# Optimization experiments

Measured on AMD Instinct MI355X. Metric: run time of the kernel, lower is better.

Reference implementation:

```python
import jax, jax.numpy as jnp
import numpy as np

K = 3
STRIDE = 1
PAD = 1
DIL = 1


def setup_inputs() -> dict:
    key = jax.random.key(0)
    k1, k2, k3, k4 = jax.random.split(key, 4)
    B, C, H, W = 8, 64, 96, 96
    O = 64
    x = jax.random.normal(k1, (B, C, H, W), jnp.float32)
    # offset-predicting conv is conventionally near-zero init -> small offsets
    w_off = jax.random.normal(k2, (2 * K * K, C, K, K), jnp.float32) * 0.01
    b_off = jax.random.normal(k3, (2 * K * K,), jnp.float32) * 0.01
    w_dcn = jax.random.normal(k4, (O, C, K, K), jnp.float32) * (1.0 / np.sqrt(C * K * K))
    return {"x": x, "w_off": w_off, "b_off": b_off, "w_dcn": w_dcn}


def _deform_conv(x, offset, w_dcn):
    B, C, H, W = x.shape
    O = w_dcn.shape[0]
    Ho, Wo = offset.shape[2], offset.shape[3]
    K2 = K * K
    # torchvision layout: offset[:, 2*k] = dy, offset[:, 2*k+1] = dx, k = ky*K + kx
    off = offset.reshape(B, K2, 2, Ho, Wo)
    kk = jnp.arange(K2)
    ky = (kk // K).astype(jnp.float32)
    kx = (kk % K).astype(jnp.float32)
    base_h = (jnp.arange(Ho) * STRIDE - PAD).astype(jnp.float32)
    base_w = (jnp.arange(Wo) * STRIDE - PAD).astype(jnp.float32)
    # sampling positions, shape [B, K2, Ho, Wo]
    py = off[:, :, 0] + base_h[None, None, :, None] + (ky * DIL)[None, :, None, None]
    px = off[:, :, 1] + base_w[None, None, None, :] + (kx * DIL)[None, :, None, None]

    y0 = jnp.floor(py)
    x0 = jnp.floor(px)
    wy = py - y0
    wx = px - x0
    y0i = y0.astype(jnp.int32)
    x0i = x0.astype(jnp.int32)
    y1i = y0i + 1
    x1i = x0i + 1

    x_flat = x.reshape(B, C, H * W)
    N = K2 * Ho * Wo

    def gather(yi, xi):
        valid = (yi >= 0) & (yi < H) & (xi >= 0) & (xi < W)
        lin = jnp.clip(yi, 0, H - 1) * W + jnp.clip(xi, 0, W - 1)  # [B,K2,Ho,Wo]
        idx = jnp.broadcast_to(lin.reshape(B, 1, N), (B, C, N))
        v = jnp.take_along_axis(x_flat, idx, axis=2).reshape(B, C, K2, Ho, Wo)
        return v * valid[:, None].astype(x.dtype)

    w00 = ((1 - wy) * (1 - wx))[:, None]
    w01 = ((1 - wy) * wx)[:, None]
    w10 = (wy * (1 - wx))[:, None]
    w11 = (wy * wx)[:, None]
    sampled = (gather(y0i, x0i) * w00 + gather(y0i, x1i) * w01
               + gather(y1i, x0i) * w10 + gather(y1i, x1i) * w11)  # [B,C,K2,Ho,Wo]

    # deformable conv = contraction over (c_in, kernel pos); bias=False
    return jnp.einsum('bckhw,ock->bohw', sampled, w_dcn.reshape(O, C, K2))


def reference(x, w_off, b_off, w_dcn):
    offset = jax.lax.conv_general_dilated(
        x, w_off, window_strides=(STRIDE, STRIDE), padding=[(PAD, PAD), (PAD, PAD)],
        rhs_dilation=(DIL, DIL), dimension_numbers=('NCHW', 'OIHW', 'NCHW'))
    offset = offset + b_off[None, :, None, None]
    return _deform_conv(x, offset, w_dcn)
```

## Files before the change

### kernel.cpp

```cpp
#include <hip/hip_runtime.h>

#define BB 8
#define CC 64
#define HH 96
#define WW 96
#define OO 64
#define KK 3
#define K2 9
#define HW (HH*WW)
#define NOFF 18
#define NPIX (BB*HW)
#define MT 64
#define NTILE (HW/MT)
#define NXCD 8
#define WR 6
#define WC 36
#define NWIN (WR*WC)
#define OSTR 21

typedef _Float16 f16;
typedef __attribute__((ext_vector_type(2))) _Float16 f16x2;
typedef __attribute__((ext_vector_type(4))) _Float16 f16x4;
typedef __attribute__((ext_vector_type(4))) float f32x4;
typedef __attribute__((ext_vector_type(2))) unsigned int uint2v;
typedef __attribute__((ext_vector_type(4))) unsigned int uint4v;

#define MFMA16(a,b,c) __builtin_amdgcn_mfma_f32_16x16x16f16(a,b,c,0,0,0)

__device__ __forceinline__ f16x2 bch(unsigned u) { return __builtin_bit_cast(f16x2, u); }
__device__ __forceinline__ unsigned bcu(f16x2 h) { return __builtin_bit_cast(unsigned, h); }
__device__ __forceinline__ f16x4 fq(unsigned a, unsigned b) {
  uint2v u = {a, b};
  return __builtin_bit_cast(f16x4, u);
}
__device__ __forceinline__ f16x4 fq2(uint2v u) { return __builtin_bit_cast(f16x4, u); }
__device__ __forceinline__ int xcd_remap(int bid, int per) {
  return (bid & 7) * per + (bid >> 3);
}

__global__ __launch_bounds__(256) void transpose_kernel(
    const float* __restrict__ x, unsigned short* __restrict__ xt) {
  int t = threadIdx.x;
  int px = xcd_remap(blockIdx.x, NPIX / 64 / NXCD) * 64 + (t & 63);
  int cg = t >> 6;
  int b = px / HW, hw = px % HW;
  const float* xp = x + (size_t)b * CC * HW + (size_t)(cg * 16) * HW + hw;
  f16 r[16];
  #pragma unroll
  for (int i = 0; i < 16; ++i) r[i] = (f16)xp[i * HW];
  uint4v v0, v1;
  #pragma unroll
  for (int q = 0; q < 4; ++q) {
    f16x2 a = {r[q*2], r[q*2+1]};       v0[q] = bcu(a);
    f16x2 bq = {r[8+q*2], r[8+q*2+1]};  v1[q] = bcu(bq);
  }
  uint4v* dst = (uint4v*)(xt + (size_t)px * CC + cg * 16);
  dst[0] = v0; dst[1] = v1;
}

__global__ void prep_kernel(const float* __restrict__ w_dcn,
                            const float* __restrict__ w_off,
                            unsigned short* __restrict__ wtx,
                            unsigned short* __restrict__ wofx) {
  int idx = blockIdx.x * 256 + threadIdx.x;
  if (idx < 36864) {
    int e = idx & 15;
    int l = (idx >> 4) & 63;
    int nb = (idx >> 10) & 3;
    int k = idx >> 12;
    int c = 16 * (l >> 4) + e;
    int o = nb * 16 + (l & 15);
    f16 h = (f16)w_dcn[(o * CC + c) * K2 + k];
    wtx[idx] = __builtin_bit_cast(unsigned short, h);
  } else {
    int i2 = idx - 36864;
    int e = i2 & 3;
    int l = (i2 >> 2) & 63;
    int q = (i2 >> 8) & 3;
    int n = (i2 >> 10) & 1;
    int kt = i2 >> 11;
    int c = q * 16 + 4 * (l >> 4) + e;
    int j = n * 16 + (l & 15);
    f16 h = (f16)((j < NOFF) ? w_off[(j * CC + c) * K2 + kt] : 0.f);
    wofx[i2] = __builtin_bit_cast(unsigned short, h);
  }
}

#define XWIN_OFF 0
#define OFFS_OFF 27648
#define ACCX_OFF 0
#define SMEM_SZ  33024

__global__ __launch_bounds__(512, 4) void fused_kernel(
    const unsigned short* __restrict__ xt,
    const unsigned short* __restrict__ wofx,
    const float* __restrict__ b_off,
    const unsigned short* __restrict__ wtx,
    float* __restrict__ out) {
  __shared__ __align__(16) char smem[SMEM_SZ];
  char* xwin = smem + XWIN_OFF;
  float* offs = (float*)(smem + OFFS_OFF);
  float* accx = (float*)(smem + ACCX_OFF);

  int t = threadIdx.x;
  int blk = xcd_remap(blockIdx.x, NPIX / MT / NXCD);
  int b = blk / NTILE;
  int ti = blk % NTILE;
  int tr = ti / 3, tc = ti % 3;
  int h0 = tr * 2, w0 = tc * 32;
  int hw0 = h0 * WW + w0;

  const char* xb = (const char*)(xt + (size_t)b * HW * CC);

  #pragma unroll
  for (int r = 0; r < 4; ++r) {
    int d = r * 512 + t;
    if (d < NWIN * 8) {
      int row = d >> 3, sg = d & 7;
      int wr_ = row / WC, wc_ = row - wr_ * WC;
      int gy = h0 - 2 + wr_;
      int gx = w0 - 2 + wc_;
      uint4v v = (uint4v){0u, 0u, 0u, 0u};
      if (((unsigned)gy < HH) && ((unsigned)gx < WW))
        v = *(const uint4v*)(xb + (size_t)((gy * WW + gx) << 7) + (sg << 4));
      *(uint4v*)&xwin[row * 128 + ((sg ^ (row & 7)) << 4)] = v;
    }
  }
  __syncthreads();

  int wv = t >> 6;
  int l  = t & 63;
  int lr = l & 15, lh = l >> 4;

  {
    int m = wv & 3, n = wv >> 2;
    int p = m * 16 + lr;
    int prow = ((p >> 5) + 1) * WC + (p & 31) + 1;
    f32x4 accO = (f32x4){0.f, 0.f, 0.f, 0.f};
    #pragma unroll
    for (int kt = 0; kt < K2; ++kt) {
      int wrow = prow + (kt / 3) * WC + (kt % 3);
      int rs = wrow & 7;
      const char* bp = (const char*)wofx + (((size_t)(kt * 2 + n) * 4) * 64 + l) * 8;
      #pragma unroll
      for (int q = 0; q < 4; ++q) {
        uint2v a2 = *(const uint2v*)&xwin[wrow * 128
                      + ((((q << 1) + (lh >> 1)) ^ rs) << 4) + ((lh & 1) << 3)];
        uint2v b2 = *(const uint2v*)(bp + (size_t)q * (64 * 8));
        accO = MFMA16(fq2(a2), fq2(b2), accO);
      }
    }
    int j = n * 16 + lr;
    if (j < NOFF) {
      float bj = b_off[j];
      #pragma unroll
      for (int r = 0; r < 4; ++r) {
        int px = m * 16 + lh * 4 + r;
        offs[px * OSTR + j] = accO[r] + bj;
      }
    }
  }
  __syncthreads();

  int grp = wv >> 2;
  int base = grp * 5;
  int cnt  = 5 - grp;
  int Ra = (wv & 3) * 16 + lr;
  int hpix = h0 + (Ra >> 5), wpix = w0 + (Ra & 31);
  int cB = lh * 32;

  unsigned po01[5], po23[5], pw01[5], pw23[5];
  unsigned emask = 0;
  #pragma unroll
  for (int i = 0; i < 5; ++i) {
    po01[i] = 0; po23[i] = 0; pw01[i] = 0; pw23[i] = 0;
    if (i < cnt) {
      int kt = base + i;
      int ky = kt / 3, kx = kt % 3;
      float py = offs[Ra * OSTR + 2 * kt]     + (float)(hpix - 1 + ky);
      float px = offs[Ra * OSTR + 2 * kt + 1] + (float)(wpix - 1 + kx);
      float y0f = floorf(py), x0f = floorf(px);
      float wy = py - y0f, wx = px - x0f;
      int y0 = (int)y0f, x0 = (int)x0f;
      int y1 = y0 + 1, x1 = x0 + 1;
      bool vy0 = (unsigned)y0 < HH, vy1 = (unsigned)y1 < HH;
      bool vx0 = (unsigned)x0 < WW, vx1 = (unsigned)x1 < WW;
      int cy0 = min(max(y0, 0), HH - 1), cy1 = min(max(y1, 0), HH - 1);
      int cx0 = min(max(x0, 0), WW - 1), cx1 = min(max(x1, 0), WW - 1);
      float g00 = (1.f - wy) * (1.f - wx) * ((vy0 && vx0) ? 1.f : 0.f);
      float g01 = (1.f - wy) * wx         * ((vy0 && vx1) ? 1.f : 0.f);
      float g10 = wy * (1.f - wx)         * ((vy1 && vx0) ? 1.f : 0.f);
      float g11 = wy * wx                 * ((vy1 && vx1) ? 1.f : 0.f);
      int ry0 = cy0 - (h0 - 2), ry1 = cy1 - (h0 - 2);
      int rx0 = cx0 - (w0 - 2), rx1 = cx1 - (w0 - 2);
      bool inw = ((unsigned)ry0 < WR) && ((unsigned)ry1 < WR) &&
                 ((unsigned)rx0 < WC) && ((unsigned)rx1 < WC);
      if (inw) {
        po01[i] = (unsigned)((ry0 * WC + rx0) << 7)
                | ((unsigned)((ry0 * WC + rx1) << 7) << 16);
        po23[i] = (unsigned)((ry1 * WC + rx0) << 7)
                | ((unsigned)((ry1 * WC + rx1) << 7) << 16);
      } else {
        po01[i] = (unsigned)(cy0 * WW + cx0)
                | ((unsigned)(cy0 * WW + cx1) << 16) | 0x80000000u;
        po23[i] = (unsigned)(cy1 * WW + cx0)
                | ((unsigned)(cy1 * WW + cx1) << 16);
        emask |= 1u << i;
      }
      f16x2 wa = {(f16)g00, (f16)g01};
      f16x2 wb = {(f16)g10, (f16)g11};
      pw01[i] = bcu(wa);
      pw23[i] = bcu(wb);
    }
  }

  f32x4 acc[4];
  #pragma unroll
  for (int nb = 0; nb < 4; ++nb) acc[nb] = (f32x4){0.f, 0.f, 0.f, 0.f};

  #define WREAD(bo, pos) (*(const uint4v*)&xwin[(bo) + ((pos) << 4)])
  if (__ballot(emask != 0) == 0ull) {
    #pragma unroll
    for (int i = 0; i < 5; ++i) {
      if (i < cnt) {
        unsigned e0 = po01[i], e1 = po23[i];
        int i0 = (int)(e0 & 0xffffu), i1 = (int)(e0 >> 16);
        int i2 = (int)(e1 & 0xffffu), i3 = (int)(e1 >> 16);
        int s0 = lh * 2;
        uint4v c0a = WREAD(i0, s0 ^ ((i0 >> 7) & 7));
        uint4v c0b = WREAD(i0, (s0 + 1) ^ ((i0 >> 7) & 7));
        uint4v c1a = WREAD(i1, s0 ^ ((i1 >> 7) & 7));
        uint4v c1b = WREAD(i1, (s0 + 1) ^ ((i1 >> 7) & 7));
        uint4v c2a = WREAD(i2, s0 ^ ((i2 >> 7) & 7));
        uint4v c2b = WREAD(i2, (s0 + 1) ^ ((i2 >> 7) & 7));
        uint4v c3a = WREAD(i3, s0 ^ ((i3 >> 7) & 7));
        uint4v c3b = WREAD(i3, (s0 + 1) ^ ((i3 >> 7) & 7));
        f16x2 wA = bch(pw01[i]), wB = bch(pw23[i]);
        f16x2 p0 = {wA[0], wA[0]}, p1 = {wA[1], wA[1]};
        f16x2 p2 = {wB[0], wB[0]}, p3 = {wB[1], wB[1]};
        uint4v pa, pb2;
        #pragma unroll
        for (int q = 0; q < 4; ++q) {
          f16x2 s  = p0 * bch(c0a[q]) + p1 * bch(c1a[q])
                   + p2 * bch(c2a[q]) + p3 * bch(c3a[q]);
          pa[q] = bcu(s);
          f16x2 s2 = p0 * bch(c0b[q]) + p1 * bch(c1b[q])
                   + p2 * bch(c2b[q]) + p3 * bch(c3b[q]);
          pb2[q] = bcu(s2);
        }
        f16x4 a0 = fq(pa[0],  pa[1]);
        f16x4 a1 = fq(pa[2],  pa[3]);
        f16x4 a2 = fq(pb2[0], pb2[1]);
        f16x4 a3 = fq(pb2[2], pb2[3]);
        const char* wbase = (const char*)wtx
                          + (((size_t)(base + i) * 4) * 64 + l) * 32;
        #pragma unroll
        for (int nb = 0; nb < 4; ++nb) {
          const char* wp = wbase + (size_t)nb * (64 * 32);
          uint4v u0 = *(const uint4v*)wp;
          uint4v u1 = *(const uint4v*)(wp + 16);
          acc[nb] = MFMA16(a0, fq(u0[0], u0[1]), acc[nb]);
          acc[nb] = MFMA16(a1, fq(u0[2], u0[3]), acc[nb]);
          acc[nb] = MFMA16(a2, fq(u1[0], u1[1]), acc[nb]);
          acc[nb] = MFMA16(a3, fq(u1[2], u1[3]), acc[nb]);
        }
      }
    }
  } else {
    #pragma unroll
    for (int i = 0; i < 5; ++i) {
      if (i < cnt) {
        unsigned e0 = po01[i], e1 = po23[i];
        uint4v c0a, c0b, c1a, c1b, c2a, c2b, c3a, c3b;
        if ((int)e0 >= 0) {
          int i0 = (int)(e0 & 0xffffu), i1 = (int)(e0 >> 16);
          int i2 = (int)(e1 & 0xffffu), i3 = (int)(e1 >> 16);
          int s0 = lh * 2;
          c0a = WREAD(i0, s0 ^ ((i0 >> 7) & 7));
          c0b = WREAD(i0, (s0 + 1) ^ ((i0 >> 7) & 7));
          c1a = WREAD(i1, s0 ^ ((i1 >> 7) & 7));
          c1b = WREAD(i1, (s0 + 1) ^ ((i1 >> 7) & 7));
          c2a = WREAD(i2, s0 ^ ((i2 >> 7) & 7));
          c2b = WREAD(i2, (s0 + 1) ^ ((i2 >> 7) & 7));
          c3a = WREAD(i3, s0 ^ ((i3 >> 7) & 7));
          c3b = WREAD(i3, (s0 + 1) ^ ((i3 >> 7) & 7));
        } else {
          int i0 = (int)(e0 & 0x7fffu) << 7;
          int i1 = (int)((e0 >> 16) & 0x7fffu) << 7;
          int i2 = (int)(e1 & 0x7fffu) << 7;
          int i3 = (int)((e1 >> 16) & 0x7fffu) << 7;
          c0a = *(const uint4v*)(xb + i0 + cB);
          c0b = *(const uint4v*)(xb + i0 + cB + 16);
          c1a = *(const uint4v*)(xb + i1 + cB);
          c1b = *(const uint4v*)(xb + i1 + cB + 16);
          c2a = *(const uint4v*)(xb + i2 + cB);
          c2b = *(const uint4v*)(xb + i2 + cB + 16);
          c3a = *(const uint4v*)(xb + i3 + cB);
          c3b = *(const uint4v*)(xb + i3 + cB + 16);
        }
        f16x2 wA = bch(pw01[i]), wB = bch(pw23[i]);
        f16x2 p0 = {wA[0], wA[0]}, p1 = {wA[1], wA[1]};
        f16x2 p2 = {wB[0], wB[0]}, p3 = {wB[1], wB[1]};
        uint4v pa, pb2;
        #pragma unroll
        for (int q = 0; q < 4; ++q) {
          f16x2 s  = p0 * bch(c0a[q]) + p1 * bch(c1a[q])
                   + p2 * bch(c2a[q]) + p3 * bch(c3a[q]);
          pa[q] = bcu(s);
          f16x2 s2 = p0 * bch(c0b[q]) + p1 * bch(c1b[q])
                   + p2 * bch(c2b[q]) + p3 * bch(c3b[q]);
          pb2[q] = bcu(s2);
        }
        f16x4 a0 = fq(pa[0],  pa[1]);
        f16x4 a1 = fq(pa[2],  pa[3]);
        f16x4 a2 = fq(pb2[0], pb2[1]);
        f16x4 a3 = fq(pb2[2], pb2[3]);
        const char* wbase = (const char*)wtx
                          + (((size_t)(base + i) * 4) * 64 + l) * 32;
        #pragma unroll
        for (int nb = 0; nb < 4; ++nb) {
          const char* wp = wbase + (size_t)nb * (64 * 32);
          uint4v u0 = *(const uint4v*)wp;
          uint4v u1 = *(const uint4v*)(wp + 16);
          acc[nb] = MFMA16(a0, fq(u0[0], u0[1]), acc[nb]);
          acc[nb] = MFMA16(a1, fq(u0[2], u0[3]), acc[nb]);
          acc[nb] = MFMA16(a2, fq(u1[0], u1[1]), acc[nb]);
          acc[nb] = MFMA16(a3, fq(u1[2], u1[3]), acc[nb]);
        }
      }
    }
  }
  __syncthreads();

  if (grp == 1) {
    #pragma unroll
    for (int nb = 0; nb < 4; ++nb)
      *(f32x4*)&accx[(nb * 16 + lr) * 68 + (wv & 3) * 16 + lh * 4] = acc[nb];
  }
  __syncthreads();
  if (grp == 0) {
    float* ob = out + (size_t)b * OO * HW;
    #pragma unroll
    for (int nb = 0; nb < 4; ++nb) {
      f32x4 other = *(const f32x4*)&accx[(nb * 16 + lr) * 68 + (wv & 3) * 16 + lh * 4];
      f32x4 v = acc[nb] + other;
      int o = nb * 16 + lr;
      int m = (wv & 3) * 16 + lh * 4;
      int base2 = hw0 + (m >> 5) * WW + (m & 31);
      *(f32x4*)(ob + (size_t)o * HW + base2) = v;
    }
  }
}

extern "C" void kernel_launch(void* const* d_in, const int* in_sizes, int n_in,
                              void* d_out, int out_size, void* d_ws, size_t ws_size,
                              hipStream_t stream) {
  const float* x     = (const float*)d_in[0];
  const float* w_off = (const float*)d_in[1];
  const float* b_off = (const float*)d_in[2];
  const float* w_dcn = (const float*)d_in[3];
  float* out = (float*)d_out;

  char* ws = (char*)d_ws;
  unsigned short* xtp  = (unsigned short*)ws;
  unsigned short* wtx  = (unsigned short*)(ws + 9437184);
  unsigned short* wofx = (unsigned short*)(ws + 9437184 + 73728);

  transpose_kernel<<<NPIX / 64, 256, 0, stream>>>(x, xtp);
  prep_kernel<<<(36864 + 18432) / 256, 256, 0, stream>>>(w_dcn, w_off, wtx, wofx);
  fused_kernel<<<NPIX / MT, 512, 0, stream>>>(xtp, wofx, b_off, wtx, out);
}
```

Baseline: 45.33 us.

## Load input window via direct global-to-LDS loads, repack offset weights, add setprio

```diff
diff --git a/kernel.cpp b/kernel.cpp
--- a/kernel.cpp
+++ b/kernel.cpp
@@ -27,6 +27,9 @@
 
 #define MFMA16(a,b,c) __builtin_amdgcn_mfma_f32_16x16x16f16(a,b,c,0,0,0)
 
+typedef const unsigned int __attribute__((address_space(1))) gau32;
+typedef unsigned int __attribute__((address_space(3))) lau32;
+
 __device__ __forceinline__ f16x2 bch(unsigned u) { return __builtin_bit_cast(f16x2, u); }
 __device__ __forceinline__ unsigned bcu(f16x2 h) { return __builtin_bit_cast(unsigned, h); }
 __device__ __forceinline__ f16x4 fq(unsigned a, unsigned b) {
@@ -61,8 +64,10 @@
 __global__ void prep_kernel(const float* __restrict__ w_dcn,
                             const float* __restrict__ w_off,
                             unsigned short* __restrict__ wtx,
-                            unsigned short* __restrict__ wofx) {
+                            unsigned short* __restrict__ wofx,
+                            unsigned short* __restrict__ zp) {
   int idx = blockIdx.x * 256 + threadIdx.x;
+  if (idx < 64) zp[idx] = 0;
   if (idx < 36864) {
     int e = idx & 15;
     int l = (idx >> 4) & 63;
@@ -74,11 +79,11 @@
     wtx[idx] = __builtin_bit_cast(unsigned short, h);
   } else {
     int i2 = idx - 36864;
-    int e = i2 & 3;
-    int l = (i2 >> 2) & 63;
-    int q = (i2 >> 8) & 3;
+    int m = i2 & 15;
+    int l = (i2 >> 4) & 63;
     int n = (i2 >> 10) & 1;
     int kt = i2 >> 11;
+    int q = m >> 2, e = m & 3;
     int c = q * 16 + 4 * (l >> 4) + e;
     int j = n * 16 + (l & 15);
     f16 h = (f16)((j < NOFF) ? w_off[(j * CC + c) * K2 + kt] : 0.f);
@@ -96,6 +101,7 @@
     const unsigned short* __restrict__ wofx,
     const float* __restrict__ b_off,
     const unsigned short* __restrict__ wtx,
+    const unsigned short* __restrict__ zp,
     float* __restrict__ out) {
   __shared__ __align__(16) char smem[SMEM_SZ];
   char* xwin = smem + XWIN_OFF;
@@ -116,14 +122,16 @@
   for (int r = 0; r < 4; ++r) {
     int d = r * 512 + t;
     if (d < NWIN * 8) {
-      int row = d >> 3, sg = d & 7;
+      int row = d >> 3, pos = d & 7;
       int wr_ = row / WC, wc_ = row - wr_ * WC;
       int gy = h0 - 2 + wr_;
       int gx = w0 - 2 + wc_;
-      uint4v v = (uint4v){0u, 0u, 0u, 0u};
-      if (((unsigned)gy < HH) && ((unsigned)gx < WW))
-        v = *(const uint4v*)(xb + (size_t)((gy * WW + gx) << 7) + (sg << 4));
-      *(uint4v*)&xwin[row * 128 + ((sg ^ (row & 7)) << 4)] = v;
+      int sg = pos ^ (row & 7);
+      const char* src = (((unsigned)gy < HH) && ((unsigned)gx < WW))
+          ? xb + (size_t)((gy * WW + gx) << 7) + (sg << 4)
+          : (const char*)zp + (sg << 4);
+      __builtin_amdgcn_global_load_lds((gau32*)src, (lau32*)(xwin + d * 16),
+                                       16, 0, 0);
     }
   }
   __syncthreads();
@@ -137,19 +145,27 @@
     int p = m * 16 + lr;
     int prow = ((p >> 5) + 1) * WC + (p & 31) + 1;
     f32x4 accO = (f32x4){0.f, 0.f, 0.f, 0.f};
+    __builtin_amdgcn_s_setprio(1);
     #pragma unroll
     for (int kt = 0; kt < K2; ++kt) {
       int wrow = prow + (kt / 3) * WC + (kt % 3);
       int rs = wrow & 7;
-      const char* bp = (const char*)wofx + (((size_t)(kt * 2 + n) * 4) * 64 + l) * 8;
+      const char* bp = (const char*)wofx + (((size_t)(kt * 2 + n)) * 64 + l) * 32;
+      uint4v bw0 = *(const uint4v*)bp;
+      uint4v bw1 = *(const uint4v*)(bp + 16);
       #pragma unroll
       for (int q = 0; q < 4; ++q) {
         uint2v a2 = *(const uint2v*)&xwin[wrow * 128
                       + ((((q << 1) + (lh >> 1)) ^ rs) << 4) + ((lh & 1) << 3)];
-        uint2v b2 = *(const uint2v*)(bp + (size_t)q * (64 * 8));
+        uint2v b2;
+        if (q == 0)      { b2[0] = bw0[0]; b2[1] = bw0[1]; }
+        else if (q == 1) { b2[0] = bw0[2]; b2[1] = bw0[3]; }
+        else if (q == 2) { b2[0] = bw1[0]; b2[1] = bw1[1]; }
+        else             { b2[0] = bw1[2]; b2[1] = bw1[3]; }
         accO = MFMA16(fq2(a2), fq2(b2), accO);
       }
     }
+    __builtin_amdgcn_s_setprio(0);
     int j = n * 16 + lr;
     if (j < NOFF) {
       float bj = b_off[j];
@@ -254,6 +270,7 @@
         f16x4 a3 = fq(pb2[2], pb2[3]);
         const char* wbase = (const char*)wtx
                           + (((size_t)(base + i) * 4) * 64 + l) * 32;
+        __builtin_amdgcn_s_setprio(1);
         #pragma unroll
         for (int nb = 0; nb < 4; ++nb) {
           const char* wp = wbase + (size_t)nb * (64 * 32);
@@ -264,6 +281,7 @@
           acc[nb] = MFMA16(a2, fq(u1[0], u1[1]), acc[nb]);
           acc[nb] = MFMA16(a3, fq(u1[2], u1[3]), acc[nb]);
         }
+        __builtin_amdgcn_s_setprio(0);
       }
     }
   } else {
@@ -365,8 +383,9 @@
   unsigned short* xtp  = (unsigned short*)ws;
   unsigned short* wtx  = (unsigned short*)(ws + 9437184);
   unsigned short* wofx = (unsigned short*)(ws + 9437184 + 73728);
+  unsigned short* zp   = (unsigned short*)(ws + 9437184 + 73728 + 36864);
 
   transpose_kernel<<<NPIX / 64, 256, 0, stream>>>(x, xtp);
-  prep_kernel<<<(36864 + 18432) / 256, 256, 0, stream>>>(w_dcn, w_off, wtx, wofx);
-  fused_kernel<<<NPIX / MT, 512, 0, stream>>>(xtp, wofx, b_off, wtx, out);
-}
+  prep_kernel<<<(36864 + 18432) / 256, 256, 0, stream>>>(w_dcn, w_off, wtx, wofx, zp);
+  fused_kernel<<<NPIX / MT, 512, 0, stream>>>(xtp, wofx, b_off, wtx, zp, out);
+}
```

Measured after the change: 42.03 us. 1.08x faster.
